# Kernel optimization log

Hardware: AMD Instinct MI355X
Metric: run time of the kernel (lower is better)

The kernel has to match this reference:

```python
import jax, jax.numpy as jnp
import numpy as np

N_NODES = 50000
E_DIM = 128
H_DIM = 256
OUT_DIM = 2
N_EDGES = 800000
NEG_SLOPE = 0.01  # nn.LeakyReLU default


def gcn_conv(x, W, b, src, dst, n):
    """PyG GCNConv: h = x @ W; add self-loops; sym-normalized scatter-add; + bias."""
    h = x @ W  # [N, H]
    loop = jnp.arange(n, dtype=src.dtype)
    s = jnp.concatenate([src, loop])
    d = jnp.concatenate([dst, loop])
    w = jnp.ones_like(s, dtype=h.dtype)
    deg = jax.ops.segment_sum(w, d, num_segments=n)  # in-degree incl. self-loop
    dis = jnp.where(deg > 0, jax.lax.rsqrt(deg), jnp.zeros_like(deg))
    norm = dis[s] * dis[d]  # [E+N]
    msg = h[s] * norm[:, None]  # gather + scale
    out = jax.ops.segment_sum(msg, d, num_segments=n)  # scatter-add to targets
    return out + b


def setup_inputs() -> dict:
    key = jax.random.key(0)
    ks = jax.random.split(key, 12)
    inp = {
        "mask_feature": jax.random.normal(ks[0], (N_NODES, E_DIM), jnp.float32),
        "feature": jax.random.normal(ks[1], (N_NODES, E_DIM), jnp.float32),
        "edge_index": jax.random.randint(ks[2], (2, N_EDGES), 0, N_NODES, jnp.int64 if jax.config.jax_enable_x64 else jnp.int32),
        "edge_type": jax.random.randint(ks[3], (N_EDGES,), 0, 2, jnp.int64 if jax.config.jax_enable_x64 else jnp.int32),
        # learned parameters
        "W_in": jax.random.normal(ks[4], (E_DIM, H_DIM), jnp.float32) * 0.05,
        "b_in": jnp.zeros((H_DIM,), jnp.float32),
        "Wg1": jax.random.normal(ks[5], (H_DIM, H_DIM), jnp.float32) * 0.05,
        "bg1": jnp.zeros((H_DIM,), jnp.float32),
        "Wg2": jax.random.normal(ks[6], (H_DIM, H_DIM), jnp.float32) * 0.05,
        "bg2": jnp.zeros((H_DIM,), jnp.float32),
        "W_out": jax.random.normal(ks[7], (H_DIM, OUT_DIM), jnp.float32) * 0.05,
        "b_out": jnp.zeros((OUT_DIM,), jnp.float32),
    }
    return inp


def reference(mask_feature, feature, edge_index, edge_type,
              W_in, b_in, Wg1, bg1, Wg2, bg2, W_out, b_out):
    src, dst = edge_index[0], edge_index[1]
    n = mask_feature.shape[0]
    # main branch
    x = jax.nn.leaky_relu(mask_feature @ W_in + b_in, NEG_SLOPE)
    x = gcn_conv(x, Wg1, bg1, src, dst, n)
    # dropout is identity at inference
    x = gcn_conv(x, Wg2, bg2, src, dst, n)
    x = x @ W_out + b_out  # [N, out_dim]
    # mask branch
    m = jax.nn.leaky_relu((feature - mask_feature) @ W_in + b_in, NEG_SLOPE)
    m = m @ W_out + b_out  # [N, out_dim]
    return x * m
```

## Files before the change

kernel.cpp:

```cpp
#include <hip/hip_runtime.h>


#define NEG_SLOPE 0.01f
constexpr int HD = 256;
constexpr int CHUNK = 2048;
constexpr int EPB = CHUNK / 256;
constexpr int BSTRIDE = 16384;

typedef __bf16 bf16x8 __attribute__((ext_vector_type(8)));
typedef unsigned short u16x8 __attribute__((ext_vector_type(8)));
typedef float f32x4 __attribute__((ext_vector_type(4)));

__device__ inline void split1(float v, unsigned short& h, unsigned short& l) {
  unsigned u = __float_as_uint(v);
  unsigned hb = u & 0xFFFF0000u;
  float lf = v - __uint_as_float(hb);
  unsigned ul = __float_as_uint(lf);
  h = (unsigned short)(hb >> 16);
  l = (unsigned short)((ul + 0x7FFFu + ((ul >> 16) & 1u)) >> 16);
}

__global__ __launch_bounds__(256) void k_prep(
    const float* __restrict__ Win, u16x8* __restrict__ Wf,
    const float* __restrict__ Wg1, const float* __restrict__ Wg2,
    const float* __restrict__ Wo, const float* __restrict__ bg1,
    const float* __restrict__ bg2, const float* __restrict__ bo,
    float* __restrict__ wb, float* __restrict__ uv, int* __restrict__ cur) {
  __shared__ float wt[256][2];
  const int bid = blockIdx.x, tid = threadIdx.x;
  if (bid < 32) {
    int f = bid * 4 + (tid >> 6);
    int lane = tid & 63;
    int nt = f >> 3, ks = (f >> 1) & 3, hl = f & 1;
    int n = nt * 16 + (lane & 15);
    int k0 = ks * 32 + (lane >> 4) * 8;
    u16x8 outv;
    #pragma unroll
    for (int j = 0; j < 8; ++j) {
      unsigned short h, l;
      split1(Win[(size_t)(k0 + j) * HD + n], h, l);
      outv[j] = hl ? l : h;
    }
    Wf[f * 64 + lane] = outv;
  } else if (bid == 32) {
    int r = tid;
    float s0 = 0.f, s1 = 0.f;
    for (int k = 0; k < 256; ++k) {
      float w = Wg2[r * 256 + k];
      s0 = fmaf(w, Wo[k * 2 + 0], s0);
      s1 = fmaf(w, Wo[k * 2 + 1], s1);
    }
    wt[r][0] = s0; wt[r][1] = s1;
    __syncthreads();
    float b0 = 0.f, b1 = 0.f;
    for (int k = 0; k < 256; ++k) {
      float w = Wg1[r * 256 + k];
      b0 = fmaf(w, wt[k][0], b0);
      b1 = fmaf(w, wt[k][1], b1);
    }
    wb[r * 2 + 0] = b0; wb[r * 2 + 1] = b1;
    if (r < 2) {
      float u = 0.f, v = 0.f;
      for (int k = 0; k < 256; ++k) {
        u = fmaf(bg1[k], wt[k][r], u);
        v = fmaf(bg2[k], Wo[k * 2 + r], v);
      }
      uv[r] = u;
      uv[2 + r] = v + bo[r];
    }
  } else {
    cur[tid] = 0;
  }
}

__global__ __launch_bounds__(256) void k_scatter(
    const int* __restrict__ src, const int* __restrict__ dst,
    int* __restrict__ cur, unsigned* __restrict__ packed, int E) {
  __shared__ int bins[256];
  __shared__ int lcur[256];
  const int t = threadIdx.x, b = blockIdx.x;
  bins[t] = 0;
  __syncthreads();
  int dl[EPB], sl[EPB];
  const int e0 = b * CHUNK;
  #pragma unroll
  for (int i = 0; i < EPB; ++i) {
    int e = e0 + i * 256 + t;
    if (e < E) {
      dl[i] = dst[e];
      sl[i] = src[e];
      atomicAdd(&bins[dl[i] >> 8], 1);
    } else {
      dl[i] = -1;
    }
  }
  __syncthreads();
  lcur[t] = atomicAdd(&cur[t], bins[t]);
  __syncthreads();
  #pragma unroll
  for (int i = 0; i < EPB; ++i) {
    if (dl[i] >= 0) {
      int bin = dl[i] >> 8;
      int pos = atomicAdd(&lcur[bin], 1);
      packed[(size_t)bin * BSTRIDE + pos] = ((unsigned)dl[i] << 16) | (unsigned)sl[i];
    }
  }
}

__device__ __forceinline__ void gemm_both(
    const float* __restrict__ mf, const float* __restrict__ fe,
    const u16x8* __restrict__ Wf, const float* __restrict__ bi,
    const float* __restrict__ wb, const float* __restrict__ Wo,
    float4* __restrict__ q, float* __restrict__ Pm, int M, int gbid,
    u16x8* stage) {
  const int tid = threadIdx.x;
  const int lane = tid & 63, wid = tid >> 6;
  const int base = gbid * 64 + wid * 16;
  int arow = base + (lane & 15);
  if (arow >= M) arow = M - 1;
  const int kb = (lane >> 4) * 8;
  const float* ap = mf + (size_t)arow * 128 + kb;
  const float* fp = fe + (size_t)arow * 128 + kb;

  bf16x8 ahi[4], alo[4], mhi[4], mlo[4];
  #pragma unroll
  for (int ks = 0; ks < 4; ++ks) {
    float x[8], y[8];
    *(float4*)&x[0] = *(const float4*)(ap + ks * 32);
    *(float4*)&x[4] = *(const float4*)(ap + ks * 32 + 4);
    *(float4*)&y[0] = *(const float4*)(fp + ks * 32);
    *(float4*)&y[4] = *(const float4*)(fp + ks * 32 + 4);
    u16x8 h, l, h2, l2;
    #pragma unroll
    for (int j = 0; j < 8; ++j) {
      unsigned short hh, ll;
      split1(x[j], hh, ll);      h[j] = hh;  l[j] = ll;
      split1(y[j] - x[j], hh, ll); h2[j] = hh; l2[j] = ll;
    }
    ahi[ks] = __builtin_bit_cast(bf16x8, h);
    alo[ks] = __builtin_bit_cast(bf16x8, l);
    mhi[ks] = __builtin_bit_cast(bf16x8, h2);
    mlo[ks] = __builtin_bit_cast(bf16x8, l2);
  }

  float s0[4] = {0,0,0,0}, s1[4] = {0,0,0,0};
  float t0[4] = {0,0,0,0}, t1[4] = {0,0,0,0};
  for (int nt = 0; nt < 16; ++nt) {
    __syncthreads();
    stage[tid * 2 + 0] = Wf[nt * 512 + tid * 2 + 0];
    stage[tid * 2 + 1] = Wf[nt * 512 + tid * 2 + 1];
    __syncthreads();
    f32x4 aM = {0,0,0,0}, aK = {0,0,0,0};
    #pragma unroll
    for (int ks = 0; ks < 4; ++ks) {
      bf16x8 bh = __builtin_bit_cast(bf16x8, stage[(ks * 2 + 0) * 64 + lane]);
      bf16x8 bl = __builtin_bit_cast(bf16x8, stage[(ks * 2 + 1) * 64 + lane]);
      aM = __builtin_amdgcn_mfma_f32_16x16x32_bf16(ahi[ks], bh, aM, 0, 0, 0);
      aM = __builtin_amdgcn_mfma_f32_16x16x32_bf16(alo[ks], bh, aM, 0, 0, 0);
      aM = __builtin_amdgcn_mfma_f32_16x16x32_bf16(ahi[ks], bl, aM, 0, 0, 0);
      aK = __builtin_amdgcn_mfma_f32_16x16x32_bf16(mhi[ks], bh, aK, 0, 0, 0);
      aK = __builtin_amdgcn_mfma_f32_16x16x32_bf16(mlo[ks], bh, aK, 0, 0, 0);
      aK = __builtin_amdgcn_mfma_f32_16x16x32_bf16(mhi[ks], bl, aK, 0, 0, 0);
    }
    const int col = nt * 16 + (lane & 15);
    const float bc = bi[col];
    const float w0 = wb[col * 2 + 0], w1 = wb[col * 2 + 1];
    const float v0 = Wo[col * 2 + 0], v1 = Wo[col * 2 + 1];
    #pragma unroll
    for (int r = 0; r < 4; ++r) {
      float a = aM[r] + bc; a = a > 0.f ? a : NEG_SLOPE * a;
      s0[r] = fmaf(a, w0, s0[r]); s1[r] = fmaf(a, w1, s1[r]);
      float m = aK[r] + bc; m = m > 0.f ? m : NEG_SLOPE * m;
      t0[r] = fmaf(m, v0, t0[r]); t1[r] = fmaf(m, v1, t1[r]);
    }
  }
  #pragma unroll
  for (int o = 1; o < 16; o <<= 1) {
    #pragma unroll
    for (int r = 0; r < 4; ++r) {
      s0[r] += __shfl_xor(s0[r], o, 16); s1[r] += __shfl_xor(s1[r], o, 16);
      t0[r] += __shfl_xor(t0[r], o, 16); t1[r] += __shfl_xor(t1[r], o, 16);
    }
  }
  if ((lane & 15) == 0) {
    #pragma unroll
    for (int r = 0; r < 4; ++r) {
      int row = base + (lane >> 4) * 4 + r;
      if (row < M) {
        float* qf = (float*)&q[row];
        qf[1] = s0[r];
        qf[2] = s1[r];
        Pm[row * 2 + 0] = t0[r];
        Pm[row * 2 + 1] = t1[r];
      }
    }
  }
}

__global__ __launch_bounds__(256) void k_p2_gemm(
    const unsigned* __restrict__ packed, const int* __restrict__ cur,
    int* __restrict__ rp, float4* __restrict__ q, int* __restrict__ csr, int N,
    const float* __restrict__ mf, const float* __restrict__ fe,
    const u16x8* __restrict__ Wf, const float* __restrict__ bi,
    const float* __restrict__ wb, const float* __restrict__ Wo,
    float* __restrict__ Pm, int NP2) {
  __shared__ u16x8 stage[512];
  __shared__ int cnt[256];
  __shared__ int sc[256];
  __shared__ int wsum[4];
  const int t = threadIdx.x;
  if ((int)blockIdx.x >= NP2) {
    gemm_both(mf, fe, Wf, bi, wb, Wo, q, Pm, N, blockIdx.x - NP2, stage);
    return;
  }
  const int B = blockIdx.x;
  const int lane = t & 63, wid = t >> 6;
  int tot = cur[t], incl = tot;
  #pragma unroll
  for (int o = 1; o < 64; o <<= 1) {
    int tmp = __shfl_up(incl, o, 64);
    if (lane >= o) incl += tmp;
  }
  if (lane == 63) wsum[wid] = incl;
  __syncthreads();
  int woff = 0;
  for (int w = 0; w < wid; ++w) woff += wsum[w];
  sc[t] = woff + incl - tot;
  __syncthreads();
  const int base = sc[B];
  const int ecnt = cur[B];
  const unsigned* pk = packed + (size_t)B * BSTRIDE;
  cnt[t] = 0;
  __syncthreads();
  for (int i = t; i < ecnt; i += 256)
    atomicAdd(&cnt[(pk[i] >> 16) & 0xFF], 1);
  __syncthreads();
  int v = cnt[t];
  incl = v;
  #pragma unroll
  for (int o = 1; o < 64; o <<= 1) {
    int tmp = __shfl_up(incl, o, 64);
    if (lane >= o) incl += tmp;
  }
  if (lane == 63) wsum[wid] = incl;
  __syncthreads();
  woff = 0;
  for (int w = 0; w < wid; ++w) woff += wsum[w];
  const int off = woff + incl - v;
  const int node = B * 256 + t;
  if (node < N) {
    rp[node] = base + off;
    ((float*)&q[node])[0] = rsqrtf((float)(v + 1));
  } else if (node == N) {
    rp[N] = base + off;
  }
  __syncthreads();
  cnt[t] = off;
  __syncthreads();
  for (int i = t; i < ecnt; i += 256) {
    unsigned pv = pk[i];
    int pos = base + atomicAdd(&cnt[(pv >> 16) & 0xFF], 1);
    csr[pos] = (int)(pv & 0xFFFFu);
  }
}

__global__ __launch_bounds__(256) void k_gather1(
    const int* __restrict__ rp, const int* __restrict__ csr,
    const float4* __restrict__ q, const float* __restrict__ uv,
    float* __restrict__ T2, int N) {
  int t = threadIdx.x;
  int n = blockIdx.x * 64 + (t >> 2);
  int l = t & 3;
  if (n >= N) return;
  int s0 = rp[n], s1 = rp[n + 1];
  float a0 = 0.f, a1 = 0.f;
  for (int j = s0 + l; j < s1; j += 4) {
    float4 qq = q[csr[j]];
    a0 = fmaf(qq.x, qq.y, a0);
    a1 = fmaf(qq.x, qq.z, a1);
  }
  a0 += __shfl_xor(a0, 1, 4); a1 += __shfl_xor(a1, 1, 4);
  a0 += __shfl_xor(a0, 2, 4); a1 += __shfl_xor(a1, 2, 4);
  if (l == 0) {
    float4 qn = q[n];
    float d = qn.x;
    T2[n * 2 + 0] = d * (d * fmaf(d, qn.y, a0) + uv[0]);
    T2[n * 2 + 1] = d * (d * fmaf(d, qn.z, a1) + uv[1]);
  }
}

__global__ __launch_bounds__(256) void k_gather2(
    const int* __restrict__ rp, const int* __restrict__ csr,
    const float* __restrict__ T2, const float4* __restrict__ q,
    const float* __restrict__ uv, const float* __restrict__ Pm,
    const float* __restrict__ bo, float* __restrict__ out, int N) {
  int t = threadIdx.x;
  int n = blockIdx.x * 64 + (t >> 2);
  int l = t & 3;
  if (n >= N) return;
  int s0 = rp[n], s1 = rp[n + 1];
  float a0 = 0.f, a1 = 0.f;
  for (int j = s0 + l; j < s1; j += 4) {
    int s = csr[j];
    float2 v = *(const float2*)&T2[s * 2];
    a0 += v.x; a1 += v.y;
  }
  a0 += __shfl_xor(a0, 1, 4); a1 += __shfl_xor(a1, 1, 4);
  a0 += __shfl_xor(a0, 2, 4); a1 += __shfl_xor(a1, 2, 4);
  if (l == 0) {
    float d = q[n].x;
    float2 tv = *(const float2*)&T2[n * 2];
    float z0 = d * (tv.x + a0) + uv[2];
    float z1 = d * (tv.y + a1) + uv[3];
    out[n * 2 + 0] = z0 * (Pm[n * 2 + 0] + bo[0]);
    out[n * 2 + 1] = z1 * (Pm[n * 2 + 1] + bo[1]);
  }
}

extern "C" void kernel_launch(void* const* d_in, const int* in_sizes, int n_in,
                              void* d_out, int out_size, void* d_ws, size_t ws_size,
                              hipStream_t stream) {
  const float* mf  = (const float*)d_in[0];
  const float* fe  = (const float*)d_in[1];
  const int*   ei  = (const int*)d_in[2];
  const float* Win = (const float*)d_in[4];
  const float* bin = (const float*)d_in[5];
  const float* Wg1 = (const float*)d_in[6];
  const float* bg1 = (const float*)d_in[7];
  const float* Wg2 = (const float*)d_in[8];
  const float* bg2 = (const float*)d_in[9];
  const float* Wo  = (const float*)d_in[10];
  const float* bo  = (const float*)d_in[11];
  float* out = (float*)d_out;

  const int ED = 128;
  const int N = in_sizes[0] / ED;
  const int E = in_sizes[3];
  const int* src = ei;
  const int* dst = ei + E;

  char* ws = (char*)d_ws;
  size_t off = 0;
  auto carve = [&](size_t bytes) {
    char* p = ws + off;
    off += (bytes + 255) & ~(size_t)255;
    return p;
  };
  int*      cur    = (int*)carve(256 * 4);
  unsigned* packed = (unsigned*)carve((size_t)256 * BSTRIDE * 4);
  int*      csr    = (int*)carve((size_t)E * 4);
  int*      rp     = (int*)carve((size_t)(N + 1) * 4);
  float4*   q      = (float4*)carve((size_t)N * 16);
  float*    T2     = (float*)carve((size_t)N * 2 * 4);
  float*    Pm     = (float*)carve((size_t)N * 2 * 4);
  float*    wb     = (float*)carve((size_t)HD * 2 * 4);
  float*    uv     = (float*)carve(4 * 4);
  u16x8*    Wf     = (u16x8*)carve((size_t)128 * 64 * 16);
  (void)ws_size; (void)n_in; (void)out_size;

  const int NB  = (E + CHUNK - 1) / CHUNK;
  const int NP2 = (N + 255) / 256;
  const int Gg  = (N + 63) / 64;

  k_prep<<<34, 256, 0, stream>>>(Win, Wf, Wg1, Wg2, Wo, bg1, bg2, bo, wb, uv, cur);
  k_scatter<<<NB, 256, 0, stream>>>(src, dst, cur, packed, E);
  k_p2_gemm<<<NP2 + Gg, 256, 0, stream>>>(packed, cur, rp, q, csr, N,
                                          mf, fe, Wf, bin, wb, Wo, Pm, NP2);
  k_gather1<<<Gg, 256, 0, stream>>>(rp, csr, q, uv, T2, N);
  k_gather2<<<Gg, 256, 0, stream>>>(rp, csr, T2, q, uv, Pm, bo, out, N);
}
```

Baseline: 97.63 us.

## Split fused CSR/GEMM kernel, register-prefetch weights, larger scatter chunks, unroll gathers

Splits the combined CSR-build plus GEMM launch into two kernels and rewrites the GEMM to double-buffer weight fragments in registers straight from global memory instead of staging through LDS with two barriers per tile. The scatter kernel now handles 8192 edges per block with a strided loop and a smaller bin stride. The gather loops are unrolled by two to keep more independent loads in flight, and the output bias is folded into Pm. In exchange, the GEMM no longer runs alongside the CSR build, which costs an extra launch and its overlap, and the smaller bin stride assumes no bin exceeds 8192 edges.

After: 110.5 us. 1.13x slower.

```diff
diff --git a/kernel.cpp b/kernel.cpp
--- a/kernel.cpp
+++ b/kernel.cpp
@@ -3,13 +3,14 @@
 
 #define NEG_SLOPE 0.01f
 constexpr int HD = 256;
-constexpr int CHUNK = 2048;
-constexpr int EPB = CHUNK / 256;
-constexpr int BSTRIDE = 16384;
+constexpr int CHUNK = 8192;
+constexpr int BSTRIDE = 8192;
 
 typedef __bf16 bf16x8 __attribute__((ext_vector_type(8)));
 typedef unsigned short u16x8 __attribute__((ext_vector_type(8)));
 typedef float f32x4 __attribute__((ext_vector_type(4)));
+
+#define MFMA16 __builtin_amdgcn_mfma_f32_16x16x32_bf16
 
 __device__ inline void split1(float v, unsigned short& h, unsigned short& l) {
   unsigned u = __float_as_uint(v);
@@ -81,138 +82,27 @@
   const int t = threadIdx.x, b = blockIdx.x;
   bins[t] = 0;
   __syncthreads();
-  int dl[EPB], sl[EPB];
-  const int e0 = b * CHUNK;
-  #pragma unroll
-  for (int i = 0; i < EPB; ++i) {
-    int e = e0 + i * 256 + t;
-    if (e < E) {
-      dl[i] = dst[e];
-      sl[i] = src[e];
-      atomicAdd(&bins[dl[i] >> 8], 1);
-    } else {
-      dl[i] = -1;
-    }
-  }
+  const int e0 = b * CHUNK, e1 = min(e0 + CHUNK, E);
+  for (int e = e0 + t; e < e1; e += 256)
+    atomicAdd(&bins[dst[e] >> 8], 1);
   __syncthreads();
   lcur[t] = atomicAdd(&cur[t], bins[t]);
   __syncthreads();
-  #pragma unroll
-  for (int i = 0; i < EPB; ++i) {
-    if (dl[i] >= 0) {
-      int bin = dl[i] >> 8;
-      int pos = atomicAdd(&lcur[bin], 1);
-      packed[(size_t)bin * BSTRIDE + pos] = ((unsigned)dl[i] << 16) | (unsigned)sl[i];
-    }
-  }
-}
-
-__device__ __forceinline__ void gemm_both(
-    const float* __restrict__ mf, const float* __restrict__ fe,
-    const u16x8* __restrict__ Wf, const float* __restrict__ bi,
-    const float* __restrict__ wb, const float* __restrict__ Wo,
-    float4* __restrict__ q, float* __restrict__ Pm, int M, int gbid,
-    u16x8* stage) {
-  const int tid = threadIdx.x;
-  const int lane = tid & 63, wid = tid >> 6;
-  const int base = gbid * 64 + wid * 16;
-  int arow = base + (lane & 15);
-  if (arow >= M) arow = M - 1;
-  const int kb = (lane >> 4) * 8;
-  const float* ap = mf + (size_t)arow * 128 + kb;
-  const float* fp = fe + (size_t)arow * 128 + kb;
-
-  bf16x8 ahi[4], alo[4], mhi[4], mlo[4];
-  #pragma unroll
-  for (int ks = 0; ks < 4; ++ks) {
-    float x[8], y[8];
-    *(float4*)&x[0] = *(const float4*)(ap + ks * 32);
-    *(float4*)&x[4] = *(const float4*)(ap + ks * 32 + 4);
-    *(float4*)&y[0] = *(const float4*)(fp + ks * 32);
-    *(float4*)&y[4] = *(const float4*)(fp + ks * 32 + 4);
-    u16x8 h, l, h2, l2;
-    #pragma unroll
-    for (int j = 0; j < 8; ++j) {
-      unsigned short hh, ll;
-      split1(x[j], hh, ll);      h[j] = hh;  l[j] = ll;
-      split1(y[j] - x[j], hh, ll); h2[j] = hh; l2[j] = ll;
-    }
-    ahi[ks] = __builtin_bit_cast(bf16x8, h);
-    alo[ks] = __builtin_bit_cast(bf16x8, l);
-    mhi[ks] = __builtin_bit_cast(bf16x8, h2);
-    mlo[ks] = __builtin_bit_cast(bf16x8, l2);
-  }
-
-  float s0[4] = {0,0,0,0}, s1[4] = {0,0,0,0};
-  float t0[4] = {0,0,0,0}, t1[4] = {0,0,0,0};
-  for (int nt = 0; nt < 16; ++nt) {
-    __syncthreads();
-    stage[tid * 2 + 0] = Wf[nt * 512 + tid * 2 + 0];
-    stage[tid * 2 + 1] = Wf[nt * 512 + tid * 2 + 1];
-    __syncthreads();
-    f32x4 aM = {0,0,0,0}, aK = {0,0,0,0};
-    #pragma unroll
-    for (int ks = 0; ks < 4; ++ks) {
-      bf16x8 bh = __builtin_bit_cast(bf16x8, stage[(ks * 2 + 0) * 64 + lane]);
-      bf16x8 bl = __builtin_bit_cast(bf16x8, stage[(ks * 2 + 1) * 64 + lane]);
-      aM = __builtin_amdgcn_mfma_f32_16x16x32_bf16(ahi[ks], bh, aM, 0, 0, 0);
-      aM = __builtin_amdgcn_mfma_f32_16x16x32_bf16(alo[ks], bh, aM, 0, 0, 0);
-      aM = __builtin_amdgcn_mfma_f32_16x16x32_bf16(ahi[ks], bl, aM, 0, 0, 0);
-      aK = __builtin_amdgcn_mfma_f32_16x16x32_bf16(mhi[ks], bh, aK, 0, 0, 0);
-      aK = __builtin_amdgcn_mfma_f32_16x16x32_bf16(mlo[ks], bh, aK, 0, 0, 0);
-      aK = __builtin_amdgcn_mfma_f32_16x16x32_bf16(mhi[ks], bl, aK, 0, 0, 0);
-    }
-    const int col = nt * 16 + (lane & 15);
-    const float bc = bi[col];
-    const float w0 = wb[col * 2 + 0], w1 = wb[col * 2 + 1];
-    const float v0 = Wo[col * 2 + 0], v1 = Wo[col * 2 + 1];
-    #pragma unroll
-    for (int r = 0; r < 4; ++r) {
-      float a = aM[r] + bc; a = a > 0.f ? a : NEG_SLOPE * a;
-      s0[r] = fmaf(a, w0, s0[r]); s1[r] = fmaf(a, w1, s1[r]);
-      float m = aK[r] + bc; m = m > 0.f ? m : NEG_SLOPE * m;
-      t0[r] = fmaf(m, v0, t0[r]); t1[r] = fmaf(m, v1, t1[r]);
-    }
-  }
-  #pragma unroll
-  for (int o = 1; o < 16; o <<= 1) {
-    #pragma unroll
-    for (int r = 0; r < 4; ++r) {
-      s0[r] += __shfl_xor(s0[r], o, 16); s1[r] += __shfl_xor(s1[r], o, 16);
-      t0[r] += __shfl_xor(t0[r], o, 16); t1[r] += __shfl_xor(t1[r], o, 16);
-    }
-  }
-  if ((lane & 15) == 0) {
-    #pragma unroll
-    for (int r = 0; r < 4; ++r) {
-      int row = base + (lane >> 4) * 4 + r;
-      if (row < M) {
-        float* qf = (float*)&q[row];
-        qf[1] = s0[r];
-        qf[2] = s1[r];
-        Pm[row * 2 + 0] = t0[r];
-        Pm[row * 2 + 1] = t1[r];
-      }
-    }
-  }
-}
-
-__global__ __launch_bounds__(256) void k_p2_gemm(
+  for (int e = e0 + t; e < e1; e += 256) {
+    int d = dst[e], s = src[e];
+    int bin = d >> 8;
+    int pos = atomicAdd(&lcur[bin], 1);
+    packed[(size_t)bin * BSTRIDE + pos] = ((unsigned)d << 16) | (unsigned)s;
+  }
+}
+
+__global__ __launch_bounds__(256) void k_p2(
     const unsigned* __restrict__ packed, const int* __restrict__ cur,
-    int* __restrict__ rp, float4* __restrict__ q, int* __restrict__ csr, int N,
-    const float* __restrict__ mf, const float* __restrict__ fe,
-    const u16x8* __restrict__ Wf, const float* __restrict__ bi,
-    const float* __restrict__ wb, const float* __restrict__ Wo,
-    float* __restrict__ Pm, int NP2) {
-  __shared__ u16x8 stage[512];
+    int* __restrict__ rp, float4* __restrict__ q, int* __restrict__ csr, int N) {
   __shared__ int cnt[256];
   __shared__ int sc[256];
   __shared__ int wsum[4];
   const int t = threadIdx.x;
-  if ((int)blockIdx.x >= NP2) {
-    gemm_both(mf, fe, Wf, bi, wb, Wo, q, Pm, N, blockIdx.x - NP2, stage);
-    return;
-  }
   const int B = blockIdx.x;
   const int lane = t & 63, wid = t >> 6;
   int tot = cur[t], incl = tot;
@@ -261,6 +151,112 @@
     unsigned pv = pk[i];
     int pos = base + atomicAdd(&cnt[(pv >> 16) & 0xFF], 1);
     csr[pos] = (int)(pv & 0xFFFFu);
+  }
+}
+
+__global__ __launch_bounds__(256) void k_gemm(
+    const float* __restrict__ mf, const float* __restrict__ fe,
+    const u16x8* __restrict__ Wf, const float* __restrict__ bi,
+    const float* __restrict__ wb, const float* __restrict__ Wo,
+    const float* __restrict__ bo, float4* __restrict__ q,
+    float* __restrict__ Pm, int M) {
+  const int tid = threadIdx.x;
+  const int lane = tid & 63, wid = tid >> 6;
+  const int base = blockIdx.x * 64 + wid * 16;
+  int arow = base + (lane & 15);
+  if (arow >= M) arow = M - 1;
+  const int kb = (lane >> 4) * 8;
+  const float* ap = mf + (size_t)arow * 128 + kb;
+  const float* fp = fe + (size_t)arow * 128 + kb;
+
+  bf16x8 ahi[4], alo[4], mhi[4], mlo[4];
+  #pragma unroll
+  for (int ks = 0; ks < 4; ++ks) {
+    float x[8], y[8];
+    *(float4*)&x[0] = *(const float4*)(ap + ks * 32);
+    *(float4*)&x[4] = *(const float4*)(ap + ks * 32 + 4);
+    *(float4*)&y[0] = *(const float4*)(fp + ks * 32);
+    *(float4*)&y[4] = *(const float4*)(fp + ks * 32 + 4);
+    u16x8 h, l, h2, l2;
+    #pragma unroll
+    for (int j = 0; j < 8; ++j) {
+      unsigned short hh, ll;
+      split1(x[j], hh, ll);        h[j] = hh;  l[j] = ll;
+      split1(y[j] - x[j], hh, ll); h2[j] = hh; l2[j] = ll;
+    }
+    ahi[ks] = __builtin_bit_cast(bf16x8, h);
+    alo[ks] = __builtin_bit_cast(bf16x8, l);
+    mhi[ks] = __builtin_bit_cast(bf16x8, h2);
+    mlo[ks] = __builtin_bit_cast(bf16x8, l2);
+  }
+
+  const u16x8* wp = Wf + lane;
+  float s0[4] = {0,0,0,0}, s1[4] = {0,0,0,0};
+  float t0[4] = {0,0,0,0}, t1[4] = {0,0,0,0};
+
+  u16x8 bA[8], bB[8];
+  #pragma unroll
+  for (int f = 0; f < 8; ++f) bA[f] = wp[f * 64];
+
+  auto COMPUTE = [&](const u16x8* b, int nt) {
+    f32x4 aM = {0,0,0,0}, aK = {0,0,0,0};
+    #pragma unroll
+    for (int ks = 0; ks < 4; ++ks) {
+      bf16x8 bh = __builtin_bit_cast(bf16x8, b[ks * 2 + 0]);
+      bf16x8 bl = __builtin_bit_cast(bf16x8, b[ks * 2 + 1]);
+      aM = MFMA16(ahi[ks], bh, aM, 0, 0, 0);
+      aM = MFMA16(alo[ks], bh, aM, 0, 0, 0);
+      aM = MFMA16(ahi[ks], bl, aM, 0, 0, 0);
+      aK = MFMA16(mhi[ks], bh, aK, 0, 0, 0);
+      aK = MFMA16(mlo[ks], bh, aK, 0, 0, 0);
+      aK = MFMA16(mhi[ks], bl, aK, 0, 0, 0);
+    }
+    const int col = nt * 16 + (lane & 15);
+    const float bc = bi[col];
+    const float w0 = wb[col * 2 + 0], w1 = wb[col * 2 + 1];
+    const float v0 = Wo[col * 2 + 0], v1 = Wo[col * 2 + 1];
+    #pragma unroll
+    for (int r = 0; r < 4; ++r) {
+      float a = aM[r] + bc; a = a > 0.f ? a : NEG_SLOPE * a;
+      s0[r] = fmaf(a, w0, s0[r]); s1[r] = fmaf(a, w1, s1[r]);
+      float m = aK[r] + bc; m = m > 0.f ? m : NEG_SLOPE * m;
+      t0[r] = fmaf(m, v0, t0[r]); t1[r] = fmaf(m, v1, t1[r]);
+    }
+  };
+
+  #pragma unroll 1
+  for (int nt = 0; nt < 16; nt += 2) {
+    #pragma unroll
+    for (int f = 0; f < 8; ++f) bB[f] = wp[((nt + 1) * 8 + f) * 64];
+    COMPUTE(bA, nt);
+    if (nt + 2 < 16) {
+      #pragma unroll
+      for (int f = 0; f < 8; ++f) bA[f] = wp[((nt + 2) * 8 + f) * 64];
+    }
+    COMPUTE(bB, nt + 1);
+  }
+
+  #pragma unroll
+  for (int o = 1; o < 16; o <<= 1) {
+    #pragma unroll
+    for (int r = 0; r < 4; ++r) {
+      s0[r] += __shfl_xor(s0[r], o, 16); s1[r] += __shfl_xor(s1[r], o, 16);
+      t0[r] += __shfl_xor(t0[r], o, 16); t1[r] += __shfl_xor(t1[r], o, 16);
+    }
+  }
+  if ((lane & 15) == 0) {
+    float bo0 = bo[0], bo1 = bo[1];
+    #pragma unroll
+    for (int r = 0; r < 4; ++r) {
+      int row = base + (lane >> 4) * 4 + r;
+      if (row < M) {
+        float* qf = (float*)&q[row];
+        qf[1] = s0[r];
+        qf[2] = s1[r];
+        Pm[row * 2 + 0] = t0[r] + bo0;
+        Pm[row * 2 + 1] = t1[r] + bo1;
+      }
+    }
   }
 }
 
@@ -274,10 +270,16 @@
   if (n >= N) return;
   int s0 = rp[n], s1 = rp[n + 1];
   float a0 = 0.f, a1 = 0.f;
-  for (int j = s0 + l; j < s1; j += 4) {
-    float4 qq = q[csr[j]];
-    a0 = fmaf(qq.x, qq.y, a0);
-    a1 = fmaf(qq.x, qq.z, a1);
+  int j = s0 + l;
+  for (; j + 4 < s1; j += 8) {
+    int sa = csr[j], sb = csr[j + 4];
+    float4 qa = q[sa], qb = q[sb];
+    a0 = fmaf(qa.x, qa.y, a0); a1 = fmaf(qa.x, qa.z, a1);
+    a0 = fmaf(qb.x, qb.y, a0); a1 = fmaf(qb.x, qb.z, a1);
+  }
+  if (j < s1) {
+    float4 qa = q[csr[j]];
+    a0 = fmaf(qa.x, qa.y, a0); a1 = fmaf(qa.x, qa.z, a1);
   }
   a0 += __shfl_xor(a0, 1, 4); a1 += __shfl_xor(a1, 1, 4);
   a0 += __shfl_xor(a0, 2, 4); a1 += __shfl_xor(a1, 2, 4);
@@ -293,17 +295,23 @@
     const int* __restrict__ rp, const int* __restrict__ csr,
     const float* __restrict__ T2, const float4* __restrict__ q,
     const float* __restrict__ uv, const float* __restrict__ Pm,
-    const float* __restrict__ bo, float* __restrict__ out, int N) {
+    float* __restrict__ out, int N) {
   int t = threadIdx.x;
   int n = blockIdx.x * 64 + (t >> 2);
   int l = t & 3;
   if (n >= N) return;
   int s0 = rp[n], s1 = rp[n + 1];
   float a0 = 0.f, a1 = 0.f;
-  for (int j = s0 + l; j < s1; j += 4) {
-    int s = csr[j];
-    float2 v = *(const float2*)&T2[s * 2];
-    a0 += v.x; a1 += v.y;
+  int j = s0 + l;
+  for (; j + 4 < s1; j += 8) {
+    int sa = csr[j], sb = csr[j + 4];
+    float2 va = *(const float2*)&T2[sa * 2];
+    float2 vb = *(const float2*)&T2[sb * 2];
+    a0 += va.x + vb.x; a1 += va.y + vb.y;
+  }
+  if (j < s1) {
+    float2 va = *(const float2*)&T2[csr[j] * 2];
+    a0 += va.x; a1 += va.y;
   }
   a0 += __shfl_xor(a0, 1, 4); a1 += __shfl_xor(a1, 1, 4);
   a0 += __shfl_xor(a0, 2, 4); a1 += __shfl_xor(a1, 2, 4);
@@ -312,8 +320,8 @@
     float2 tv = *(const float2*)&T2[n * 2];
     float z0 = d * (tv.x + a0) + uv[2];
     float z1 = d * (tv.y + a1) + uv[3];
-    out[n * 2 + 0] = z0 * (Pm[n * 2 + 0] + bo[0]);
-    out[n * 2 + 1] = z1 * (Pm[n * 2 + 1] + bo[1]);
+    out[n * 2 + 0] = z0 * Pm[n * 2 + 0];
+    out[n * 2 + 1] = z1 * Pm[n * 2 + 1];
   }
 }
 
@@ -364,8 +372,8 @@
 
   k_prep<<<34, 256, 0, stream>>>(Win, Wf, Wg1, Wg2, Wo, bg1, bg2, bo, wb, uv, cur);
   k_scatter<<<NB, 256, 0, stream>>>(src, dst, cur, packed, E);
-  k_p2_gemm<<<NP2 + Gg, 256, 0, stream>>>(packed, cur, rp, q, csr, N,
-                                          mf, fe, Wf, bin, wb, Wo, Pm, NP2);
+  k_p2<<<NP2, 256, 0, stream>>>(packed, cur, rp, q, csr, N);
+  k_gemm<<<Gg, 256, 0, stream>>>(mf, fe, Wf, bin, wb, Wo, bo, q, Pm, N);
   k_gather1<<<Gg, 256, 0, stream>>>(rp, csr, q, uv, T2, N);
-  k_gather2<<<Gg, 256, 0, stream>>>(rp, csr, T2, q, uv, Pm, bo, out, N);
-}
+  k_gather2<<<Gg, 256, 0, stream>>>(rp, csr, T2, q, uv, Pm, out, N);
+}
```
